# Performance work log

Hardware: AMD Instinct MI355X
Metric: run time of the kernel (lower is better)

## Reference

```python
import jax, jax.numpy as jnp
import numpy as np

B, N, E = 16, 1024, 32768
D_IN, HID, HEADS, OUT = 33, 32, 4, 8  # OUT = d_mid // heads
EPS = 1e-5
NEG_SLOPE = 0.2  # PyG GATConv default leaky_relu slope


def layer_norm(x, g, b):
    m = x.mean(-1, keepdims=True)
    v = ((x - m) ** 2).mean(-1, keepdims=True)
    return (x - m) / jnp.sqrt(v + EPS) * g + b


def gat_conv(x, src, dst, W, a_src, a_dst, bias):
    # x: [N, F_in]; W: [F_in, HEADS*OUT]; a_src/a_dst: [HEADS, OUT]
    n = x.shape[0]
    xp = (x @ W).reshape(n, HEADS, OUT)                 # [N, H, D]
    al_s = (xp * a_src).sum(-1)                          # [N, H]
    al_d = (xp * a_dst).sum(-1)                          # [N, H]
    e = jax.nn.leaky_relu(al_s[src] + al_d[dst], NEG_SLOPE)  # [E, H]
    # softmax over incoming edges per target node (PyG: softmax over edge_index[1])
    m = jax.ops.segment_max(e, dst, num_segments=n)
    ex = jnp.exp(e - m[dst])
    s = jax.ops.segment_sum(ex, dst, num_segments=n)
    alpha = ex / s[dst]                                  # [E, H]
    out = jax.ops.segment_sum(xp[src] * alpha[:, :, None], dst, num_segments=n)
    return out.reshape(n, HEADS * OUT) + bias, alpha


def setup_inputs() -> dict:
    key = jax.random.key(0)
    ks = jax.random.split(key, 16)
    inp = {
        "H": jax.random.normal(ks[0], (B, N, D_IN), jnp.float32),
        "edge_index": jax.random.randint(ks[1], (2, E), 0, N, dtype=jnp.int64),
        # ObsEmbedding params
        "W1_e": jax.random.normal(ks[2], (D_IN, HID), jnp.float32) * 0.1,
        "b1_e": jnp.zeros((HID,), jnp.float32),
        "W2_e": jax.random.normal(ks[3], (HID, HID), jnp.float32) * 0.1,
        "b2_e": jnp.zeros((HID,), jnp.float32),
        "ln_e_g": jnp.ones((HID,), jnp.float32),
        "ln_e_b": jnp.zeros((HID,), jnp.float32),
        # GAT1 params
        "W_g1": jax.random.normal(ks[4], (HID, HEADS * OUT), jnp.float32) * 0.1,
        "as_g1": jax.random.normal(ks[5], (HEADS, OUT), jnp.float32) * 0.1,
        "ad_g1": jax.random.normal(ks[6], (HEADS, OUT), jnp.float32) * 0.1,
        "bi_g1": jnp.zeros((HEADS * OUT,), jnp.float32),
        # GAT2 params
        "W_g2": jax.random.normal(ks[7], (HEADS * OUT, HEADS * OUT), jnp.float32) * 0.1,
        "as_g2": jax.random.normal(ks[8], (HEADS, OUT), jnp.float32) * 0.1,
        "ad_g2": jax.random.normal(ks[9], (HEADS, OUT), jnp.float32) * 0.1,
        "bi_g2": jnp.zeros((HEADS * OUT,), jnp.float32),
        # output LayerNorm
        "ln_o_g": jnp.ones((HEADS * OUT,), jnp.float32),
        "ln_o_b": jnp.zeros((HEADS * OUT,), jnp.float32),
    }
    return inp


def reference(H, edge_index, W1_e, b1_e, W2_e, b2_e, ln_e_g, ln_e_b,
              W_g1, as_g1, ad_g1, bi_g1, W_g2, as_g2, ad_g2, bi_g2,
              ln_o_g, ln_o_b):
    src, dst = edge_index[0], edge_index[1]

    # ObsEmbedding: Linear->ReLU->Linear->ReLU->LayerNorm (batched, dense)
    x = jax.nn.relu(H @ W1_e + b1_e)
    x = jax.nn.relu(x @ W2_e + b2_e)
    x = layer_norm(x, ln_e_g, ln_e_b)          # [B, N, 32]

    def per_graph(xb):
        h1, _ = gat_conv(xb, src, dst, W_g1, as_g1, ad_g1, bi_g1)
        h1 = jax.nn.relu(h1)
        h2, alpha2 = gat_conv(h1, src, dst, W_g2, as_g2, ad_g2, bi_g2)
        h_out = layer_norm(h1 + h2, ln_o_g, ln_o_b)
        return h_out, alpha2

    h_out, alpha2 = jax.vmap(per_graph)(x)      # [B, N, 32], [B, E, HEADS]

    # scatter edge attention into dense [B, HEADS, N, N] at [src, dst]
    alpha_t = jnp.transpose(alpha2, (0, 2, 1))  # [B, HEADS, E]
    A = jnp.zeros((B, HEADS, N, N), jnp.float32).at[:, :, src, dst].set(alpha_t)
    return h_out, A
```

## Files before the change

kernel.cpp:

```cpp
#include <hip/hip_runtime.h>
#include <hip/hip_bf16.h>

#define BB 16
#define NN 1024
#define EE 32768
#define D_IN 33
#define HID 32
#define HEADS 4
#define OUTD 8
#define FF 32
#define EPSL 1e-5f
#define SLOPE 0.2f

__device__ __forceinline__ float red32(float v) {
    v += __shfl_xor(v, 1);
    v += __shfl_xor(v, 2);
    v += __shfl_xor(v, 4);
    v += __shfl_xor(v, 8);
    v += __shfl_xor(v, 16);
    return v;
}
__device__ __forceinline__ float red8(float v) {
    v += __shfl_xor(v, 1);
    v += __shfl_xor(v, 2);
    v += __shfl_xor(v, 4);
    return v;
}

__global__ __launch_bounds__(256) void k_init(int* __restrict__ deg,
                                              int* __restrict__ deg2) {
    int i = threadIdx.x;
    for (int k = i; k < NN; k += 256) { deg[k] = 0; deg2[k] = 0; }
}

__global__ __launch_bounds__(256) void k_count(const int* __restrict__ ei,
                                               int* __restrict__ deg,
                                               int* __restrict__ deg2) {
    int e = blockIdx.x * 256 + threadIdx.x;
    if (e < EE) {
        atomicAdd(&deg[ei[EE + e]], 1);
        atomicAdd(&deg2[ei[e]], 1);
    }
}

__global__ __launch_bounds__(1024) void k_scan(
    const int* __restrict__ deg, int* __restrict__ off, int* __restrict__ cur,
    const int* __restrict__ deg2, int* __restrict__ off2, int* __restrict__ cur2) {
    __shared__ int tmp[NN];
    int t = threadIdx.x;
    tmp[t] = deg[t];
    __syncthreads();
    for (int s = 1; s < NN; s <<= 1) {
        int v = (t >= s) ? tmp[t - s] : 0;
        __syncthreads();
        tmp[t] += v;
        __syncthreads();
    }
    off[t + 1] = tmp[t];
    if (t == 0) off[0] = 0;
    cur[t] = (t == 0) ? 0 : tmp[t - 1];
    __syncthreads();
    tmp[t] = deg2[t];
    __syncthreads();
    for (int s = 1; s < NN; s <<= 1) {
        int v = (t >= s) ? tmp[t - s] : 0;
        __syncthreads();
        tmp[t] += v;
        __syncthreads();
    }
    off2[t + 1] = tmp[t];
    if (t == 0) off2[0] = 0;
    cur2[t] = (t == 0) ? 0 : tmp[t - 1];
}

__global__ __launch_bounds__(256) void k_fill(const int* __restrict__ ei,
                                              int* __restrict__ cur,
                                              int* __restrict__ csr_src,
                                              int* __restrict__ csr_eid,
                                              int* __restrict__ cur2,
                                              int* __restrict__ out_dst,
                                              int* __restrict__ out_eid) {
    int e = blockIdx.x * 256 + threadIdx.x;
    if (e < EE) {
        int s = ei[e], d = ei[EE + e];
        int p = atomicAdd(&cur[d], 1);
        csr_src[p] = s;
        csr_eid[p] = e;
        int p2 = atomicAdd(&cur2[s], 1);
        out_dst[p2] = d;
        out_eid[p2] = e;
    }
}

__global__ __launch_bounds__(256) void k_embed(
    const float* __restrict__ Hm, const float* __restrict__ W1,
    const float* __restrict__ b1, const float* __restrict__ W2,
    const float* __restrict__ b2, const float* __restrict__ lng,
    const float* __restrict__ lnb, const float* __restrict__ Wg1,
    const float* __restrict__ as1, const float* __restrict__ ad1,
    float* __restrict__ xp1, float* __restrict__ als1, float* __restrict__ ald1) {
    __shared__ float sW1[D_IN * 32];
    __shared__ float sW2[32 * 32];
    __shared__ float sWg[32 * 32];
    __shared__ float sb1[32], sb2[32], sg[32], sbt[32], sas[32], sad[32];
    __shared__ float sh[8][34];
    __shared__ float sx[8][33];
    int tid = threadIdx.x;
    for (int i = tid; i < D_IN * 32; i += 256) sW1[i] = W1[i];
    for (int i = tid; i < 1024; i += 256) { sW2[i] = W2[i]; sWg[i] = Wg1[i]; }
    if (tid < 32) {
        sb1[tid] = b1[tid]; sb2[tid] = b2[tid];
        sg[tid] = lng[tid]; sbt[tid] = lnb[tid];
        sas[tid] = as1[tid]; sad[tid] = ad1[tid];
    }
    int g = tid >> 5, j = tid & 31;
    int idx = blockIdx.x * 8 + g;
    __syncthreads();
    int base = idx * D_IN;
    for (int i = j; i < D_IN; i += 32) sh[g][i] = Hm[base + i];
    __syncthreads();
    float acc = sb1[j];
#pragma unroll
    for (int i = 0; i < D_IN; i++) acc += sh[g][i] * sW1[i * 32 + j];
    float x1 = fmaxf(acc, 0.f);
    sx[g][j] = x1;
    __syncthreads();
    acc = sb2[j];
#pragma unroll
    for (int i = 0; i < 32; i++) acc += sx[g][i] * sW2[i * 32 + j];
    float x2 = fmaxf(acc, 0.f);
    float mean = red32(x2) * (1.f / 32.f);
    float d0 = x2 - mean;
    float var = red32(d0 * d0) * (1.f / 32.f);
    float xn = d0 * rsqrtf(var + EPSL) * sg[j] + sbt[j];
    __syncthreads();
    sx[g][j] = xn;
    __syncthreads();
    acc = 0.f;
#pragma unroll
    for (int i = 0; i < 32; i++) acc += sx[g][i] * sWg[i * 32 + j];
    xp1[idx * 32 + j] = acc;
    float ps = red8(acc * sas[j]);
    float pd = red8(acc * sad[j]);
    if ((j & 7) == 0) {
        als1[idx * 4 + (j >> 3)] = ps;
        ald1[idx * 4 + (j >> 3)] = pd;
    }
}

__global__ __launch_bounds__(256) void k_gat1(
    const int* __restrict__ off, const int* __restrict__ csr_src,
    const float* __restrict__ xp1, const float* __restrict__ als1,
    const float* __restrict__ ald1, const float* __restrict__ bi1,
    const float* __restrict__ Wg2, const float* __restrict__ as2,
    const float* __restrict__ ad2, float* __restrict__ h1,
    float* __restrict__ xp2, float* __restrict__ als2, float* __restrict__ ald2) {
    __shared__ float sW[1024];
    __shared__ float sb[32], sas[32], sad[32];
    __shared__ float sx[8][33];
    int tid = threadIdx.x;
    for (int i = tid; i < 1024; i += 256) sW[i] = Wg2[i];
    if (tid < 32) { sb[tid] = bi1[tid]; sas[tid] = as2[tid]; sad[tid] = ad2[tid]; }
    __syncthreads();
    int g = tid >> 5, j = tid & 31, h = j >> 3, lane8 = j & 7;
    int idx = blockIdx.x * 8 + g;
    int b = idx >> 10, n = idx & 1023;
    int beg = off[n], end = off[n + 1];
    float aldh = ald1[idx * 4 + h];
    const float* alsb = als1 + b * NN * 4;
    float se = 0.f;
    for (int k = beg + lane8; k < end; k += 8) {
        int s = csr_src[k];
        float av = alsb[s * 4 + h] + aldh;
        av = av > 0.f ? av : SLOPE * av;
        se += __expf(av);
    }
    se = red8(se);
    float inv = se > 0.f ? 1.f / se : 0.f;
    const float* xpb = xp1 + b * NN * 32;
    float acc = 0.f;
    for (int kb = beg; kb < end; kb += 8) {
        int k = kb + lane8;
        float al = 0.f;
        int s = 0;
        if (k < end) {
            s = csr_src[k];
            float av = alsb[s * 4 + h] + aldh;
            av = av > 0.f ? av : SLOPE * av;
            al = __expf(av) * inv;
        }
        int lim = end - kb; if (lim > 8) lim = 8;
        for (int t = 0; t < lim; t++) {
            int st = __shfl(s, t, 32);
            float alt = __shfl(al, (h << 3) + t, 32);
            acc += alt * xpb[st * 32 + j];
        }
    }
    float hv = fmaxf(acc + sb[j], 0.f);
    h1[idx * 32 + j] = hv;
    sx[g][j] = hv;
    __syncthreads();
    float x2 = 0.f;
#pragma unroll
    for (int i = 0; i < 32; i++) x2 += sx[g][i] * sW[i * 32 + j];
    xp2[idx * 32 + j] = x2;
    float ps = red8(x2 * sas[j]);
    float pd = red8(x2 * sad[j]);
    if ((j & 7) == 0) { als2[idx * 4 + h] = ps; ald2[idx * 4 + h] = pd; }
}

__global__ __launch_bounds__(256) void k_gat2(
    const int* __restrict__ off, const int* __restrict__ csr_src,
    const int* __restrict__ csr_eid, const float* __restrict__ xp2,
    const float* __restrict__ als2, const float* __restrict__ ald2,
    const float* __restrict__ h1, const float* __restrict__ bi2,
    const float* __restrict__ lng, const float* __restrict__ lnb,
    float* __restrict__ outH, float* __restrict__ alphaE) {
    __shared__ float sb[32], sg[32], sbt[32];
    int tid = threadIdx.x;
    if (tid < 32) { sb[tid] = bi2[tid]; sg[tid] = lng[tid]; sbt[tid] = lnb[tid]; }
    __syncthreads();
    int g = tid >> 5, j = tid & 31, h = j >> 3, lane8 = j & 7;
    int idx = blockIdx.x * 8 + g;
    int b = idx >> 10, n = idx & 1023;
    int beg = off[n], end = off[n + 1];
    float aldh = ald2[idx * 4 + h];
    const float* alsb = als2 + b * NN * 4;
    float se = 0.f;
    for (int k = beg + lane8; k < end; k += 8) {
        int s = csr_src[k];
        float av = alsb[s * 4 + h] + aldh;
        av = av > 0.f ? av : SLOPE * av;
        se += __expf(av);
    }
    se = red8(se);
    float inv = se > 0.f ? 1.f / se : 0.f;
    const float* xpb = xp2 + b * NN * 32;
    float* aEb = alphaE + (size_t)b * 4 * EE + (size_t)h * EE;
    float acc = 0.f;
    for (int kb = beg; kb < end; kb += 8) {
        int k = kb + lane8;
        float al = 0.f;
        int s = 0;
        if (k < end) {
            s = csr_src[k];
            float av = alsb[s * 4 + h] + aldh;
            av = av > 0.f ? av : SLOPE * av;
            al = __expf(av) * inv;
            aEb[csr_eid[k]] = al;
        }
        int lim = end - kb; if (lim > 8) lim = 8;
        for (int t = 0; t < lim; t++) {
            int st = __shfl(s, t, 32);
            float alt = __shfl(al, (h << 3) + t, 32);
            acc += alt * xpb[st * 32 + j];
        }
    }
    float y = h1[idx * 32 + j] + acc + sb[j];
    float mean = red32(y) * (1.f / 32.f);
    float d0 = y - mean;
    float var = red32(d0 * d0) * (1.f / 32.f);
    outH[idx * 32 + j] = d0 * rsqrtf(var + EPSL) * sg[j] + sbt[j];
}

#define ROWS_PER_BLOCK 4
__global__ __launch_bounds__(256) void k_rowA(
    const int* __restrict__ off2, const int* __restrict__ out_dst,
    const int* __restrict__ out_eid, const float* __restrict__ alphaE,
    float* __restrict__ A) {
    __shared__ float sRow[ROWS_PER_BLOCK][NN];
    int wid = threadIdx.x >> 6, lane = threadIdx.x & 63;
    int r = blockIdx.x * ROWS_PER_BLOCK + wid;
    int bh = r >> 10, src = r & 1023;
    float4* row4 = (float4*)&sRow[wid][0];
    float4 z = make_float4(0.f, 0.f, 0.f, 0.f);
#pragma unroll
    for (int i = 0; i < 4; i++) row4[i * 64 + lane] = z;
    __syncthreads();
    int beg = off2[src], end = off2[src + 1];
    const float* aE = alphaE + (size_t)bh * EE;
    for (int p = beg + lane; p < end; p += 64) {
        sRow[wid][out_dst[p]] = aE[out_eid[p]];
    }
    __syncthreads();
    float4* o4 = (float4*)(A + (size_t)bh * (NN * NN) + (size_t)src * NN);
#pragma unroll
    for (int i = 0; i < 4; i++) o4[i * 64 + lane] = row4[i * 64 + lane];
}

extern "C" void kernel_launch(void* const* d_in, const int* in_sizes, int n_in,
                              void* d_out, int out_size, void* d_ws, size_t ws_size,
                              hipStream_t stream) {
    const float* Hm  = (const float*)d_in[0];
    const int*   ei  = (const int*)d_in[1];
    const float* W1  = (const float*)d_in[2];
    const float* b1  = (const float*)d_in[3];
    const float* W2  = (const float*)d_in[4];
    const float* b2  = (const float*)d_in[5];
    const float* lneg = (const float*)d_in[6];
    const float* lneb = (const float*)d_in[7];
    const float* Wg1 = (const float*)d_in[8];
    const float* as1 = (const float*)d_in[9];
    const float* ad1 = (const float*)d_in[10];
    const float* bi1 = (const float*)d_in[11];
    const float* Wg2 = (const float*)d_in[12];
    const float* as2 = (const float*)d_in[13];
    const float* ad2 = (const float*)d_in[14];
    const float* bi2 = (const float*)d_in[15];
    const float* lnog = (const float*)d_in[16];
    const float* lnob = (const float*)d_in[17];

    float* outH = (float*)d_out;
    float* A    = outH + BB * NN * FF;

    int* deg     = (int*)d_ws;
    int* off     = deg + 1024;
    int* cur     = off + 1028;
    int* deg2    = cur + 1024;
    int* off2    = deg2 + 1024;
    int* cur2    = off2 + 1028;
    int* csr_src = cur2 + 1024;
    int* csr_eid = csr_src + EE;
    int* out_dst = csr_eid + EE;
    int* out_eid = out_dst + EE;
    float* fb    = (float*)(out_eid + EE);
    float* xp1    = fb;
    float* als1   = xp1 + BB * NN * FF;
    float* ald1   = als1 + BB * NN * 4;
    float* h1     = ald1 + BB * NN * 4;
    float* xp2    = h1 + BB * NN * FF;
    float* als2   = xp2 + BB * NN * FF;
    float* ald2   = als2 + BB * NN * 4;
    float* alphaE = ald2 + BB * NN * 4;

    hipLaunchKernelGGL(k_init, dim3(1), dim3(256), 0, stream, deg, deg2);
    hipLaunchKernelGGL(k_count, dim3(EE / 256), dim3(256), 0, stream, ei, deg, deg2);
    hipLaunchKernelGGL(k_scan, dim3(1), dim3(1024), 0, stream,
                       deg, off, cur, deg2, off2, cur2);
    hipLaunchKernelGGL(k_fill, dim3(EE / 256), dim3(256), 0, stream,
                       ei, cur, csr_src, csr_eid, cur2, out_dst, out_eid);
    hipLaunchKernelGGL(k_embed, dim3(BB * NN / 8), dim3(256), 0, stream,
                       Hm, W1, b1, W2, b2, lneg, lneb, Wg1, as1, ad1,
                       xp1, als1, ald1);
    hipLaunchKernelGGL(k_gat1, dim3(BB * NN / 8), dim3(256), 0, stream,
                       off, csr_src, xp1, als1, ald1, bi1, Wg2, as2, ad2,
                       h1, xp2, als2, ald2);
    hipLaunchKernelGGL(k_gat2, dim3(BB * NN / 8), dim3(256), 0, stream,
                       off, csr_src, csr_eid, xp2, als2, ald2, h1, bi2, lnog, lnob,
                       outH, alphaE);
    hipLaunchKernelGGL(k_rowA, dim3(BB * HEADS * NN / ROWS_PER_BLOCK), dim3(256),
                       0, stream, off2, out_dst, out_eid, alphaE, A);
}
```

Baseline: 409.3 us.

## Store edge attention in source-sorted order and stage gather operands in LDS

```diff
diff --git a/kernel.cpp b/kernel.cpp
--- a/kernel.cpp
+++ b/kernel.cpp
@@ -76,19 +76,17 @@
 __global__ __launch_bounds__(256) void k_fill(const int* __restrict__ ei,
                                               int* __restrict__ cur,
                                               int* __restrict__ csr_src,
-                                              int* __restrict__ csr_eid,
                                               int* __restrict__ cur2,
                                               int* __restrict__ out_dst,
-                                              int* __restrict__ out_eid) {
+                                              int* __restrict__ csr_opos) {
     int e = blockIdx.x * 256 + threadIdx.x;
     if (e < EE) {
         int s = ei[e], d = ei[EE + e];
         int p = atomicAdd(&cur[d], 1);
         csr_src[p] = s;
-        csr_eid[p] = e;
         int p2 = atomicAdd(&cur2[s], 1);
         out_dst[p2] = d;
-        out_eid[p2] = e;
+        csr_opos[p] = p2;
     }
 }
 
@@ -158,18 +156,20 @@
     __shared__ float sW[1024];
     __shared__ float sb[32], sas[32], sad[32];
     __shared__ float sx[8][33];
+    __shared__ float salp[8][32];
+    __shared__ int   ssrc[8][8];
     int tid = threadIdx.x;
     for (int i = tid; i < 1024; i += 256) sW[i] = Wg2[i];
     if (tid < 32) { sb[tid] = bi1[tid]; sas[tid] = as2[tid]; sad[tid] = ad2[tid]; }
     __syncthreads();
-    int g = tid >> 5, j = tid & 31, h = j >> 3, lane8 = j & 7;
+    int g = tid >> 5, j = tid & 31, h = j >> 3, t8 = j & 7;
     int idx = blockIdx.x * 8 + g;
     int b = idx >> 10, n = idx & 1023;
     int beg = off[n], end = off[n + 1];
     float aldh = ald1[idx * 4 + h];
     const float* alsb = als1 + b * NN * 4;
     float se = 0.f;
-    for (int k = beg + lane8; k < end; k += 8) {
+    for (int k = beg + t8; k < end; k += 8) {
         int s = csr_src[k];
         float av = alsb[s * 4 + h] + aldh;
         av = av > 0.f ? av : SLOPE * av;
@@ -180,21 +180,21 @@
     const float* xpb = xp1 + b * NN * 32;
     float acc = 0.f;
     for (int kb = beg; kb < end; kb += 8) {
-        int k = kb + lane8;
-        float al = 0.f;
-        int s = 0;
+        int k = kb + t8;
+        float al = 0.f; int s = 0;
         if (k < end) {
             s = csr_src[k];
             float av = alsb[s * 4 + h] + aldh;
             av = av > 0.f ? av : SLOPE * av;
             al = __expf(av) * inv;
         }
-        int lim = end - kb; if (lim > 8) lim = 8;
-        for (int t = 0; t < lim; t++) {
-            int st = __shfl(s, t, 32);
-            float alt = __shfl(al, (h << 3) + t, 32);
-            acc += alt * xpb[st * 32 + j];
-        }
+        salp[g][j] = al;
+        if (h == 0) ssrc[g][t8] = s;
+        __builtin_amdgcn_wave_barrier();
+#pragma unroll
+        for (int t = 0; t < 8; t++)
+            acc += salp[g][(h << 3) + t] * xpb[ssrc[g][t] * 32 + j];
+        __builtin_amdgcn_wave_barrier();
     }
     float hv = fmaxf(acc + sb[j], 0.f);
     h1[idx * 32 + j] = hv;
@@ -211,23 +211,25 @@
 
 __global__ __launch_bounds__(256) void k_gat2(
     const int* __restrict__ off, const int* __restrict__ csr_src,
-    const int* __restrict__ csr_eid, const float* __restrict__ xp2,
+    const int* __restrict__ csr_opos, const float* __restrict__ xp2,
     const float* __restrict__ als2, const float* __restrict__ ald2,
     const float* __restrict__ h1, const float* __restrict__ bi2,
     const float* __restrict__ lng, const float* __restrict__ lnb,
     float* __restrict__ outH, float* __restrict__ alphaE) {
     __shared__ float sb[32], sg[32], sbt[32];
+    __shared__ float salp[8][32];
+    __shared__ int   ssrc[8][8];
     int tid = threadIdx.x;
     if (tid < 32) { sb[tid] = bi2[tid]; sg[tid] = lng[tid]; sbt[tid] = lnb[tid]; }
     __syncthreads();
-    int g = tid >> 5, j = tid & 31, h = j >> 3, lane8 = j & 7;
+    int g = tid >> 5, j = tid & 31, h = j >> 3, t8 = j & 7;
     int idx = blockIdx.x * 8 + g;
     int b = idx >> 10, n = idx & 1023;
     int beg = off[n], end = off[n + 1];
     float aldh = ald2[idx * 4 + h];
     const float* alsb = als2 + b * NN * 4;
     float se = 0.f;
-    for (int k = beg + lane8; k < end; k += 8) {
+    for (int k = beg + t8; k < end; k += 8) {
         int s = csr_src[k];
         float av = alsb[s * 4 + h] + aldh;
         av = av > 0.f ? av : SLOPE * av;
@@ -236,25 +238,25 @@
     se = red8(se);
     float inv = se > 0.f ? 1.f / se : 0.f;
     const float* xpb = xp2 + b * NN * 32;
-    float* aEb = alphaE + (size_t)b * 4 * EE + (size_t)h * EE;
+    float* aEb = alphaE + ((size_t)b * 4 + h) * EE;
     float acc = 0.f;
     for (int kb = beg; kb < end; kb += 8) {
-        int k = kb + lane8;
-        float al = 0.f;
-        int s = 0;
+        int k = kb + t8;
+        float al = 0.f; int s = 0;
         if (k < end) {
             s = csr_src[k];
             float av = alsb[s * 4 + h] + aldh;
             av = av > 0.f ? av : SLOPE * av;
             al = __expf(av) * inv;
-            aEb[csr_eid[k]] = al;
+            aEb[csr_opos[k]] = al;
         }
-        int lim = end - kb; if (lim > 8) lim = 8;
-        for (int t = 0; t < lim; t++) {
-            int st = __shfl(s, t, 32);
-            float alt = __shfl(al, (h << 3) + t, 32);
-            acc += alt * xpb[st * 32 + j];
-        }
+        salp[g][j] = al;
+        if (h == 0) ssrc[g][t8] = s;
+        __builtin_amdgcn_wave_barrier();
+#pragma unroll
+        for (int t = 0; t < 8; t++)
+            acc += salp[g][(h << 3) + t] * xpb[ssrc[g][t] * 32 + j];
+        __builtin_amdgcn_wave_barrier();
     }
     float y = h1[idx * 32 + j] + acc + sb[j];
     float mean = red32(y) * (1.f / 32.f);
@@ -266,8 +268,7 @@
 #define ROWS_PER_BLOCK 4
 __global__ __launch_bounds__(256) void k_rowA(
     const int* __restrict__ off2, const int* __restrict__ out_dst,
-    const int* __restrict__ out_eid, const float* __restrict__ alphaE,
-    float* __restrict__ A) {
+    const float* __restrict__ alphaE, float* __restrict__ A) {
     __shared__ float sRow[ROWS_PER_BLOCK][NN];
     int wid = threadIdx.x >> 6, lane = threadIdx.x & 63;
     int r = blockIdx.x * ROWS_PER_BLOCK + wid;
@@ -276,13 +277,12 @@
     float4 z = make_float4(0.f, 0.f, 0.f, 0.f);
 #pragma unroll
     for (int i = 0; i < 4; i++) row4[i * 64 + lane] = z;
-    __syncthreads();
+    __builtin_amdgcn_wave_barrier();
     int beg = off2[src], end = off2[src + 1];
     const float* aE = alphaE + (size_t)bh * EE;
-    for (int p = beg + lane; p < end; p += 64) {
-        sRow[wid][out_dst[p]] = aE[out_eid[p]];
-    }
-    __syncthreads();
+    for (int p = beg + lane; p < end; p += 64)
+        sRow[wid][out_dst[p]] = aE[p];
+    __builtin_amdgcn_wave_barrier();
     float4* o4 = (float4*)(A + (size_t)bh * (NN * NN) + (size_t)src * NN);
 #pragma unroll
     for (int i = 0; i < 4; i++) o4[i * 64 + lane] = row4[i * 64 + lane];
@@ -313,17 +313,16 @@
     float* outH = (float*)d_out;
     float* A    = outH + BB * NN * FF;
 
-    int* deg     = (int*)d_ws;
-    int* off     = deg + 1024;
-    int* cur     = off + 1028;
-    int* deg2    = cur + 1024;
-    int* off2    = deg2 + 1024;
-    int* cur2    = off2 + 1028;
-    int* csr_src = cur2 + 1024;
-    int* csr_eid = csr_src + EE;
-    int* out_dst = csr_eid + EE;
-    int* out_eid = out_dst + EE;
-    float* fb    = (float*)(out_eid + EE);
+    int* deg      = (int*)d_ws;
+    int* off      = deg + 1024;
+    int* cur      = off + 1028;
+    int* deg2     = cur + 1024;
+    int* off2     = deg2 + 1024;
+    int* cur2     = off2 + 1028;
+    int* csr_src  = cur2 + 1024;
+    int* csr_opos = csr_src + EE;
+    int* out_dst  = csr_opos + EE;
+    float* fb     = (float*)(out_dst + EE);
     float* xp1    = fb;
     float* als1   = xp1 + BB * NN * FF;
     float* ald1   = als1 + BB * NN * 4;
@@ -338,7 +337,7 @@
     hipLaunchKernelGGL(k_scan, dim3(1), dim3(1024), 0, stream,
                        deg, off, cur, deg2, off2, cur2);
     hipLaunchKernelGGL(k_fill, dim3(EE / 256), dim3(256), 0, stream,
-                       ei, cur, csr_src, csr_eid, cur2, out_dst, out_eid);
+                       ei, cur, csr_src, cur2, out_dst, csr_opos);
     hipLaunchKernelGGL(k_embed, dim3(BB * NN / 8), dim3(256), 0, stream,
                        Hm, W1, b1, W2, b2, lneg, lneb, Wg1, as1, ad1,
                        xp1, als1, ald1);
@@ -346,8 +345,8 @@
                        off, csr_src, xp1, als1, ald1, bi1, Wg2, as2, ad2,
                        h1, xp2, als2, ald2);
     hipLaunchKernelGGL(k_gat2, dim3(BB * NN / 8), dim3(256), 0, stream,
-                       off, csr_src, csr_eid, xp2, als2, ald2, h1, bi2, lnog, lnob,
+                       off, csr_src, csr_opos, xp2, als2, ald2, h1, bi2, lnog, lnob,
                        outH, alphaE);
     hipLaunchKernelGGL(k_rowA, dim3(BB * HEADS * NN / ROWS_PER_BLOCK), dim3(256),
-                       0, stream, off2, out_dst, out_eid, alphaE, A);
-}
+                       0, stream, off2, out_dst, alphaE, A);
+}
```

After: 396.3 us. -3.2%, faster.
